# Performance work log

Measured on AMD Instinct MI355X. Metric: run time of the kernel, lower is better.

## Reference

```python
import jax, jax.numpy as jnp
import numpy as np


def setup_inputs() -> dict:
    key = jax.random.key(0)
    k1, k2, k3, k4 = jax.random.split(key, 4)
    B, S, H = 4, 2048, 1024
    Ha, P = 1024, 1024
    x = jax.random.normal(k1, (B, S, H), dtype=jnp.float32)
    score_weights = jax.random.normal(k2, (B, S, S), dtype=jnp.float32)
    W_c = jax.random.normal(k3, (H, 3 * Ha), dtype=jnp.float32) * 0.02
    b_c = jnp.zeros((3 * Ha,), dtype=jnp.float32)
    W_p = jax.random.normal(k4, (Ha, P), dtype=jnp.float32) * 0.02
    b_p = jnp.zeros((P,), dtype=jnp.float32)
    return {"x": x, "score_weights": score_weights, "W_c": W_c, "b_c": b_c, "W_p": W_p, "b_p": b_p}


def reference(x, score_weights, W_c, b_c, W_p, b_p):
    # fused QKV projection: [B,S,H] @ [H,3*Ha] + b -> [B,S,3*Ha]
    c = jnp.einsum("bsh,hf->bsf", x, W_c) + b_c
    Ha = c.shape[-1] // 3
    query, key, value = jnp.split(c, 3, axis=2)  # each [B,S,Ha]
    # scaled dot-product scores [B,S,S] with additive bias
    scale = jax.lax.rsqrt(jnp.asarray(Ha, dtype=x.dtype))
    scores = jnp.einsum("bqd,bkd->bqk", query, key) * scale + score_weights
    probs = jax.nn.softmax(scores, axis=-1)
    context = jnp.einsum("bqk,bkd->bqd", probs, value)  # [B,S,Ha]
    # output projection [B,S,Ha] @ [Ha,P] + b -> [B,S,P]
    return jnp.einsum("bsd,dp->bsp", context, W_p) + b_p
```

## Files before the change

### kernel.cpp

```cpp
#include <hip/hip_runtime.h>
#include <hip/hip_bf16.h>
#include <cstdint>

typedef __attribute__((ext_vector_type(8))) short v8s;
typedef __attribute__((ext_vector_type(4))) float v4f;

__device__ __forceinline__ unsigned short f32_to_bf16(float f) {
  unsigned int u = __builtin_bit_cast(unsigned int, f);
  u += 0x7fffu + ((u >> 16) & 1u);
  return (unsigned short)(u >> 16);
}

__device__ __forceinline__ void gload_lds16(const void* g, void* l) {
  __builtin_amdgcn_global_load_lds((const __attribute__((address_space(1))) void*)g,
                                   (__attribute__((address_space(3))) void*)l, 16, 0, 0);
}

enum { EPI_BF16_BIAS = 0, EPI_F32_BIAS = 1, EPI_F32_SCALE_ADD = 2 };

template <int MODE>
__global__ __launch_bounds__(256)
void gemm_nt(const unsigned short* __restrict__ A, long long strideA, int lda,
             const unsigned short* __restrict__ B, long long strideB, int ldb,
             void* __restrict__ Cout, long long strideC, int ldc,
             const float* __restrict__ bias,
             const float* __restrict__ addmat, long long strideAdd,
             float scale, int K,
             unsigned short* __restrict__ VtOut)
{
  __shared__ __attribute__((aligned(16))) short smA[128 * 64];
  __shared__ __attribute__((aligned(16))) short smB[128 * 64];

  const int tid  = threadIdx.x;
  const int lane = tid & 63;
  const int wave = tid >> 6;
  const int wm = wave >> 1, wn = wave & 1;
  const int bz = blockIdx.z;
  const int tileM = blockIdx.y * 128, tileN = blockIdx.x * 128;

  const unsigned short* Ag = A + (long long)bz * strideA + (long long)tileM * lda;
  const unsigned short* Bg = B + (long long)bz * strideB + (long long)tileN * ldb;

  const int l8    = lane >> 3;
  const int srcCb = (lane & 7) ^ l8;

  v4f acc[4][4] = {};

  for (int k0 = 0; k0 < K; k0 += 64) {
    #pragma unroll
    for (int i = 0; i < 4; ++i) {
      const int c   = wave * 4 + i;
      const int row = c * 8 + l8;
      gload_lds16(Ag + (long long)row * lda + k0 + srcCb * 8, &smA[c * 512]);
      gload_lds16(Bg + (long long)row * ldb + k0 + srcCb * 8, &smB[c * 512]);
    }
    __syncthreads();
    #pragma unroll
    for (int kk = 0; kk < 2; ++kk) {
      v8s af[4], bf[4];
      #pragma unroll
      for (int f = 0; f < 4; ++f) {
        const int rA = wm * 64 + f * 16 + (lane & 15);
        const int cA = (kk * 4 + (lane >> 4)) ^ (rA & 7);
        af[f] = *(const v8s*)&smA[rA * 64 + cA * 8];
        const int rB = wn * 64 + f * 16 + (lane & 15);
        const int cB = (kk * 4 + (lane >> 4)) ^ (rB & 7);
        bf[f] = *(const v8s*)&smB[rB * 64 + cB * 8];
      }
      #pragma unroll
      for (int fm = 0; fm < 4; ++fm)
        #pragma unroll
        for (int fn = 0; fn < 4; ++fn)
          acc[fm][fn] = __builtin_amdgcn_mfma_f32_16x16x32_bf16(af[fm], bf[fn], acc[fm][fn], 0, 0, 0);
    }
    __syncthreads();
  }

  const int row0 = tileM + wm * 64 + (lane >> 4) * 4;
  const int col0 = tileN + wn * 64 + (lane & 15);
  const bool vtActive = (MODE == EPI_BF16_BIAS) && (VtOut != nullptr) && (tileN >= 2048);

  #pragma unroll
  for (int fm = 0; fm < 4; ++fm) {
    #pragma unroll
    for (int fn = 0; fn < 4; ++fn) {
      const int col = col0 + fn * 16;
      if (vtActive) {
        const int rowb = row0 + fm * 16;
        const int d = col - 2048;
        const int b = rowb >> 11;
        const int s0 = rowb & 2047;
        const float bb = bias[col];
        ushort4 w;
        w.x = f32_to_bf16(acc[fm][fn][0] + bb);
        w.y = f32_to_bf16(acc[fm][fn][1] + bb);
        w.z = f32_to_bf16(acc[fm][fn][2] + bb);
        w.w = f32_to_bf16(acc[fm][fn][3] + bb);
        *(ushort4*)&VtOut[((long long)b * 1024 + d) * 2048 + s0] = w;
      } else {
        #pragma unroll
        for (int r = 0; r < 4; ++r) {
          const int row = row0 + fm * 16 + r;
          const float v = acc[fm][fn][r];
          if (MODE == EPI_F32_SCALE_ADD) {
            float* C = (float*)Cout + (long long)bz * strideC;
            const float* Wt = addmat + (long long)bz * strideAdd;
            C[(long long)row * ldc + col] = v * scale + Wt[(long long)row * ldc + col];
          } else if (MODE == EPI_F32_BIAS) {
            float* C = (float*)Cout + (long long)bz * strideC;
            C[(long long)row * ldc + col] = v + bias[col];
          } else {
            unsigned short* C = (unsigned short*)Cout + (long long)bz * strideC;
            const float b = bias ? bias[col] : 0.0f;
            C[(long long)row * ldc + col] = f32_to_bf16(v + b);
          }
        }
      }
    }
  }
}

__global__ __launch_bounds__(256)
void cvt_f32_bf16_kernel(const float* __restrict__ in, unsigned short* __restrict__ out,
                         long long n)
{
  const long long i = ((long long)blockIdx.x * 256 + threadIdx.x) * 4;
  if (i >= n) return;
  const float4 v = *(const float4*)(in + i);
  typedef __attribute__((ext_vector_type(4))) unsigned short v4us;
  v4us o;
  o.x = f32_to_bf16(v.x); o.y = f32_to_bf16(v.y);
  o.z = f32_to_bf16(v.z); o.w = f32_to_bf16(v.w);
  *(v4us*)(out + i) = o;
}

__global__ __launch_bounds__(256)
void transpose_f32_bf16_kernel(const float* __restrict__ in, unsigned short* __restrict__ out,
                               int R, int C)
{
  __shared__ float t[32][33];
  const int c0 = blockIdx.x * 32, r0 = blockIdx.y * 32;
  const int tx = threadIdx.x, ty = threadIdx.y;
  for (int i = ty; i < 32; i += 8)
    t[i][tx] = in[(long long)(r0 + i) * C + (c0 + tx)];
  __syncthreads();
  for (int i = ty; i < 32; i += 8)
    out[(long long)(c0 + i) * R + (r0 + tx)] = f32_to_bf16(t[tx][i]);
}

__global__ __launch_bounds__(256)
void softmax_rows(const float* __restrict__ scores, unsigned short* __restrict__ probs)
{
  const long long row = blockIdx.x;
  const float* src = scores + row * 2048;
  unsigned short* dst = probs + row * 2048;
  const int t = threadIdx.x;
  float v[8];
  const float4 a = *(const float4*)(src + t * 8);
  const float4 b = *(const float4*)(src + t * 8 + 4);
  v[0]=a.x; v[1]=a.y; v[2]=a.z; v[3]=a.w; v[4]=b.x; v[5]=b.y; v[6]=b.z; v[7]=b.w;

  float m = v[0];
  #pragma unroll
  for (int j = 1; j < 8; ++j) m = fmaxf(m, v[j]);
  for (int o = 32; o; o >>= 1) m = fmaxf(m, __shfl_xor(m, o));
  __shared__ float redm[4], reds[4];
  if ((t & 63) == 0) redm[t >> 6] = m;
  __syncthreads();
  m = fmaxf(fmaxf(redm[0], redm[1]), fmaxf(redm[2], redm[3]));

  float s = 0.f;
  #pragma unroll
  for (int j = 0; j < 8; ++j) { v[j] = __expf(v[j] - m); s += v[j]; }
  for (int o = 32; o; o >>= 1) s += __shfl_xor(s, o);
  if ((t & 63) == 0) reds[t >> 6] = s;
  __syncthreads();
  s = reds[0] + reds[1] + reds[2] + reds[3];
  const float inv = 1.0f / s;

  v8s o8;
  #pragma unroll
  for (int j = 0; j < 8; ++j) o8[j] = (short)f32_to_bf16(v[j] * inv);
  *(v8s*)(dst + t * 8) = o8;
}

extern "C" void kernel_launch(void* const* d_in, const int* in_sizes, int n_in,
                              void* d_out, int out_size, void* d_ws, size_t ws_size,
                              hipStream_t stream) {
  (void)in_sizes; (void)n_in; (void)out_size; (void)ws_size;
  const float* x   = (const float*)d_in[0];
  const float* sw  = (const float*)d_in[1];
  const float* W_c = (const float*)d_in[2];
  const float* b_c = (const float*)d_in[3];
  const float* W_p = (const float*)d_in[4];
  const float* b_p = (const float*)d_in[5];
  float* out = (float*)d_out;

  const int Bb = 4, S = 2048, H = 1024, Ha = 1024, P = 1024;
  const int M = Bb * S;
  char* ws = (char*)d_ws;
  const long long MB = 1024LL * 1024LL;
  float*          scores = (float*)(ws + 0);
  unsigned short* x_bf   = (unsigned short*)(ws + 0);
  unsigned short* ctx    = (unsigned short*)(ws + 0);
  unsigned short* probs  = (unsigned short*)(ws + 64 * MB);
  unsigned short* qkv    = (unsigned short*)(ws + 96 * MB);
  unsigned short* Vt     = (unsigned short*)(ws + 144 * MB);
  unsigned short* Wc_t   = (unsigned short*)(ws + 160 * MB);
  unsigned short* Wp_t   = (unsigned short*)(ws + 166 * MB);

  const dim3 tb(32, 8);

  cvt_f32_bf16_kernel<<<(unsigned)((long long)M * H / 4 / 256), 256, 0, stream>>>(
      x, x_bf, (long long)M * H);
  transpose_f32_bf16_kernel<<<dim3(3 * Ha / 32, H / 32), tb, 0, stream>>>(W_c, Wc_t, H, 3 * Ha);
  transpose_f32_bf16_kernel<<<dim3(P / 32, Ha / 32), tb, 0, stream>>>(W_p, Wp_t, Ha, P);
  gemm_nt<EPI_BF16_BIAS><<<dim3(3 * Ha / 128, M / 128, 1), 256, 0, stream>>>(
      x_bf, 0, H, Wc_t, 0, H, qkv, 0, 3 * Ha, b_c, nullptr, 0, 0.f, H, Vt);
  gemm_nt<EPI_F32_SCALE_ADD><<<dim3(S / 128, S / 128, Bb), 256, 0, stream>>>(
      qkv, (long long)S * 3 * Ha, 3 * Ha,
      qkv + Ha, (long long)S * 3 * Ha, 3 * Ha,
      scores, (long long)S * S, S, nullptr, sw, (long long)S * S, 0.03125f, Ha, nullptr);
  softmax_rows<<<Bb * S, 256, 0, stream>>>(scores, probs);
  gemm_nt<EPI_BF16_BIAS><<<dim3(Ha / 128, S / 128, Bb), 256, 0, stream>>>(
      probs, (long long)S * S, S, Vt, (long long)Ha * S, S,
      ctx, (long long)S * Ha, Ha, nullptr, nullptr, 0, 0.f, S, nullptr);
  gemm_nt<EPI_F32_BIAS><<<dim3(P / 128, M / 128, 1), 256, 0, stream>>>(
      ctx, 0, Ha, Wp_t, 0, Ha, out, 0, P, b_p, nullptr, 0, 0.f, Ha, nullptr);
}
```

Baseline: 260.4 us.

## Store attention scores in bf16 and remap workgroups across XCDs

The scores GEMM now writes scale-plus-bias logits as bf16 instead of fp32, and the softmax reads bf16 input. This halves the intermediate scores traffic between those two kernels. Separately, the GEMM remaps its flat workgroup index so consecutive tiles land on the same XCD, aiming for better L2 reuse. Rounding logits to bf16 before softmax adds precision error.

```diff
diff --git a/kernel.cpp b/kernel.cpp
--- a/kernel.cpp
+++ b/kernel.cpp
@@ -10,13 +10,16 @@
   u += 0x7fffu + ((u >> 16) & 1u);
   return (unsigned short)(u >> 16);
 }
+__device__ __forceinline__ float bf16_to_f32(unsigned short u) {
+  return __builtin_bit_cast(float, (unsigned int)u << 16);
+}
 
 __device__ __forceinline__ void gload_lds16(const void* g, void* l) {
   __builtin_amdgcn_global_load_lds((const __attribute__((address_space(1))) void*)g,
                                    (__attribute__((address_space(3))) void*)l, 16, 0, 0);
 }
 
-enum { EPI_BF16_BIAS = 0, EPI_F32_BIAS = 1, EPI_F32_SCALE_ADD = 2 };
+enum { EPI_BF16_BIAS = 0, EPI_F32_BIAS = 1, EPI_BF16_SCALE_ADD = 2 };
 
 template <int MODE>
 __global__ __launch_bounds__(256)
@@ -36,7 +39,12 @@
   const int wave = tid >> 6;
   const int wm = wave >> 1, wn = wave & 1;
   const int bz = blockIdx.z;
-  const int tileM = blockIdx.y * 128, tileN = blockIdx.x * 128;
+
+  const int nx  = gridDim.x;
+  const int nwg = nx * gridDim.y;
+  int h = blockIdx.x + nx * blockIdx.y;
+  if ((nwg & 7) == 0) h = (h & 7) * (nwg >> 3) + (h >> 3);
+  const int tileM = (h / nx) * 128, tileN = (h % nx) * 128;
 
   const unsigned short* Ag = A + (long long)bz * strideA + (long long)tileM * lda;
   const unsigned short* Bg = B + (long long)bz * strideB + (long long)tileN * ldb;
@@ -102,10 +110,11 @@
         for (int r = 0; r < 4; ++r) {
           const int row = row0 + fm * 16 + r;
           const float v = acc[fm][fn][r];
-          if (MODE == EPI_F32_SCALE_ADD) {
-            float* C = (float*)Cout + (long long)bz * strideC;
+          if (MODE == EPI_BF16_SCALE_ADD) {
+            unsigned short* C = (unsigned short*)Cout + (long long)bz * strideC;
             const float* Wt = addmat + (long long)bz * strideAdd;
-            C[(long long)row * ldc + col] = v * scale + Wt[(long long)row * ldc + col];
+            C[(long long)row * ldc + col] =
+                f32_to_bf16(v * scale + Wt[(long long)row * ldc + col]);
           } else if (MODE == EPI_F32_BIAS) {
             float* C = (float*)Cout + (long long)bz * strideC;
             C[(long long)row * ldc + col] = v + bias[col];
@@ -149,16 +158,17 @@
 }
 
 __global__ __launch_bounds__(256)
-void softmax_rows(const float* __restrict__ scores, unsigned short* __restrict__ probs)
+void softmax_rows_bf16(const unsigned short* __restrict__ scores,
+                       unsigned short* __restrict__ probs)
 {
   const long long row = blockIdx.x;
-  const float* src = scores + row * 2048;
+  const unsigned short* src = scores + row * 2048;
   unsigned short* dst = probs + row * 2048;
   const int t = threadIdx.x;
+  const v8s in = *(const v8s*)(src + t * 8);
   float v[8];
-  const float4 a = *(const float4*)(src + t * 8);
-  const float4 b = *(const float4*)(src + t * 8 + 4);
-  v[0]=a.x; v[1]=a.y; v[2]=a.z; v[3]=a.w; v[4]=b.x; v[5]=b.y; v[6]=b.z; v[7]=b.w;
+  #pragma unroll
+  for (int j = 0; j < 8; ++j) v[j] = bf16_to_f32((unsigned short)in[j]);
 
   float m = v[0];
   #pragma unroll
@@ -200,7 +210,7 @@
   const int M = Bb * S;
   char* ws = (char*)d_ws;
   const long long MB = 1024LL * 1024LL;
-  float*          scores = (float*)(ws + 0);
+  unsigned short* scores = (unsigned short*)(ws + 0);
   unsigned short* x_bf   = (unsigned short*)(ws + 0);
   unsigned short* ctx    = (unsigned short*)(ws + 0);
   unsigned short* probs  = (unsigned short*)(ws + 64 * MB);
@@ -217,11 +227,11 @@
   transpose_f32_bf16_kernel<<<dim3(P / 32, Ha / 32), tb, 0, stream>>>(W_p, Wp_t, Ha, P);
   gemm_nt<EPI_BF16_BIAS><<<dim3(3 * Ha / 128, M / 128, 1), 256, 0, stream>>>(
       x_bf, 0, H, Wc_t, 0, H, qkv, 0, 3 * Ha, b_c, nullptr, 0, 0.f, H, Vt);
-  gemm_nt<EPI_F32_SCALE_ADD><<<dim3(S / 128, S / 128, Bb), 256, 0, stream>>>(
+  gemm_nt<EPI_BF16_SCALE_ADD><<<dim3(S / 128, S / 128, Bb), 256, 0, stream>>>(
       qkv, (long long)S * 3 * Ha, 3 * Ha,
       qkv + Ha, (long long)S * 3 * Ha, 3 * Ha,
       scores, (long long)S * S, S, nullptr, sw, (long long)S * S, 0.03125f, Ha, nullptr);
-  softmax_rows<<<Bb * S, 256, 0, stream>>>(scores, probs);
+  softmax_rows_bf16<<<Bb * S, 256, 0, stream>>>(scores, probs);
   gemm_nt<EPI_BF16_BIAS><<<dim3(Ha / 128, S / 128, Bb), 256, 0, stream>>>(
       probs, (long long)S * S, S, Vt, (long long)Ha * S, S,
       ctx, (long long)S * Ha, Ha, nullptr, nullptr, 0, 0.f, S, nullptr);
```

New measurement: 247.6 us. 4.9% less time.
